# Optimization experiments

Hardware: AMD Instinct MI355X
Metric: run time of the kernel (lower is better)

## Reference

```python
import jax, jax.numpy as jnp
import numpy as np

N = 8192        # nodes in batch
E = 262144      # edges (avg degree 32)
IN_C = 64
OUT_C = 64
K = 3           # max_k
G = 64          # graphs in batch
NC = 10         # n_class
EPS = 1e-5      # batchnorm eps


def setup_inputs() -> dict:
    key = jax.random.key(0)
    ks = jax.random.split(key, 16)
    D_in = IN_C * K    # 192
    D_out = OUT_C * K  # 192
    inp = {
        'x': jax.random.normal(ks[0], (N, IN_C), jnp.float32),
        'edge_index': jax.random.randint(ks[1], (2, E), 0, N, dtype=jnp.int64),
        'batch': jnp.sort(jax.random.randint(ks[2], (N,), 0, G, dtype=jnp.int64)),
        # spectral-normed masked linear
        'W_orig': jax.random.normal(ks[3], (D_out, D_in), jnp.float32) * 0.05,
        'b': jnp.zeros((D_out,), jnp.float32),
        'u': jax.random.normal(ks[4], (D_out,), jnp.float32),
        # batchnorms (training-mode batch stats)
        'bn1_gamma': jnp.ones((D_out,), jnp.float32),
        'bn1_beta': jnp.zeros((D_out,), jnp.float32),
        'bn2_gamma': jnp.ones((D_out * 3,), jnp.float32),
        'bn2_beta': jnp.zeros((D_out * 3,), jnp.float32),
        # funnel head
        'w1': jax.random.normal(ks[5], (D_out * 2, D_out * 3), jnp.float32) * 0.05,
        'b1': jnp.zeros((D_out * 2,), jnp.float32),
        'w2': jax.random.normal(ks[6], (D_out, D_out * 2), jnp.float32) * 0.05,
        'b2': jnp.zeros((D_out,), jnp.float32),
        'w3': jax.random.normal(ks[7], (NC, D_out), jnp.float32) * 0.05,
        'b3': jnp.zeros((NC,), jnp.float32),
    }
    return inp


def _forward(x, edge_index, batch, W_orig, b, u, bn1_gamma, bn1_beta,
             bn2_gamma, bn2_beta, w1, b1, w2, b2, w3, b3):
    n = x.shape[0]
    row, col = edge_index[0], edge_index[1]
    # sym-normalized Laplacian L = I - D^-1/2 A D^-1/2, densified ([N,N])
    deg = jnp.zeros((n,), x.dtype).at[row].add(1.0)
    dinv = jnp.where(deg > 0, jax.lax.rsqrt(jnp.maximum(deg, 1.0)), 0.0)
    vals = -dinv[row] * dinv[col]
    L = jnp.zeros((n, n), x.dtype).at[row, col].add(vals)
    idx = jnp.arange(n)
    L = L.at[idx, idx].add(1.0)
    Hs = [x]
    h = x
    for _ in range(K - 1):
        h = L @ h
        Hs.append(h)
    Hcat = jnp.concatenate(Hs, axis=1)              # [N, IN_C*K]
    # spectral norm of W (one power-iteration step with stored u)
    v = W_orig.T @ u
    v = v / (jnp.linalg.norm(v) + 1e-12)
    sigma = u @ (W_orig @ v)
    W = W_orig / sigma
    # block lower-triangular mask: block i passes first IN_C*(i+1) input cols
    col_idx = jnp.arange(IN_C * K)
    row_block = jnp.arange(OUT_C * K) // OUT_C
    mask = (col_idx[None, :] < IN_C * (row_block[:, None] + 1)).astype(W.dtype)
    H = Hcat @ (W * mask).T + b                     # masked linear
    # reservoir_act_fun is identity (default)
    mu, var = H.mean(0), H.var(0)                   # BN (batch stats)
    H = bn1_gamma * (H - mu) * jax.lax.rsqrt(var + EPS) + bn1_beta
    # fused-style triple pooling over graph ids
    Hsum = jax.ops.segment_sum(H, batch, num_segments=G)
    cnt = jax.ops.segment_sum(jnp.ones((n,), H.dtype), batch, num_segments=G)
    Havg = Hsum / jnp.maximum(cnt, 1.0)[:, None]
    Hmax = jax.ops.segment_max(H, batch, num_segments=G)
    Hg = jnp.concatenate([Havg, Hsum, Hmax], axis=1)  # [G, 3*OUT_C*K]
    mu2, var2 = Hg.mean(0), Hg.var(0)
    xo = bn2_gamma * (Hg - mu2) * jax.lax.rsqrt(var2 + EPS) + bn2_beta
    # funnel output (dropout = identity in eval)
    xo = jax.nn.relu(xo @ w1.T + b1)
    xo = jax.nn.relu(xo @ w2.T + b2)
    return jax.nn.log_softmax(xo @ w3.T + b3, axis=1)


def reference(x, edge_index, batch, W_orig, b, u, bn1_gamma, bn1_beta,
              bn2_gamma, bn2_beta, w1, b1, w2, b2, w3, b3):
    return _forward(x, edge_index, batch, W_orig, b, u, bn1_gamma, bn1_beta,
                    bn2_gamma, bn2_beta, w1, b1, w2, b2, w3, b3)
```

## Files before the change

### kernel.cpp

```cpp
#include <hip/hip_runtime.h>
#include <math.h>

#define NN   8192
#define EE   262144
#define CIN  64
#define DD   192
#define GG   64
#define NCLS 10
#define D3   576
#define F1   384
#define F2   192
#define EPSB 1e-5f
#define NB   64
#define EPB  (EE / NB)
#define PS   8

__global__ __launch_bounds__(1024) void prep_kernel(const float* __restrict__ W,
    const float* __restrict__ u, const float* __restrict__ w1,
    const float* __restrict__ w2, const int* __restrict__ batch,
    float* __restrict__ sig, int* __restrict__ gstart,
    float* __restrict__ Wp, float* __restrict__ Wp1, float* __restrict__ Wp2) {
    int b = blockIdx.x, t = threadIdx.x;
    if (b < 324) {
        int idx = b * 1024 + t;
        if (idx < DD * DD) {
            int r = idx / DD, c = idx - r * DD;
            float m = (c < CIN * ((r >> 6) + 1)) ? 1.f : 0.f;
            Wp[((c >> 2) * DD + r) * 4 + (c & 3)] = m * W[idx];
        } else if (idx < DD * DD + F1 * D3) {
            int i1 = idx - DD * DD;
            int tt = i1 / D3, k = i1 - tt * D3;
            Wp1[((k >> 2) * F1 + tt) * 4 + (k & 3)] = w1[i1];
        } else {
            int i2 = idx - DD * DD - F1 * D3;
            int tt = i2 / F1, k = i2 - tt * F1;
            Wp2[((k >> 2) * F2 + tt) * 4 + (k & 3)] = w2[i2];
        }
        return;
    }
    if (b == 325) {
        for (int i = t; i < NN; i += 1024) {
            int b0 = batch[i];
            int b1 = (i + 1 < NN) ? batch[i + 1] : GG;
            if (i == 0) { for (int g = 0; g <= b0; g++) gstart[g] = 0; }
            for (int g = b0 + 1; g <= b1; g++) gstart[g] = i + 1;
        }
        return;
    }
    __shared__ float vp[768];
    __shared__ float vsh[DD];
    __shared__ float red[1024];
    if (t < 768) {
        int c = t >> 2, j = t & 3;
        float s = 0.f;
        const float* Wc = W + c;
        for (int i = j * 48; i < j * 48 + 48; i++) s += Wc[i * DD] * u[i];
        vp[t] = s;
    }
    __syncthreads();
    float vv = 0.f;
    if (t < DD) {
        float v = vp[4 * t] + vp[4 * t + 1] + vp[4 * t + 2] + vp[4 * t + 3];
        vsh[t] = v;
        vv = v * v;
    }
    red[t] = vv;
    __syncthreads();
    for (int off = 512; off > 0; off >>= 1) {
        if (t < off) red[t] += red[t + off];
        __syncthreads();
    }
    float norm = sqrtf(red[0]) + 1e-12f;
    __syncthreads();
    float a = 0.f;
    for (int idx = t; idx < DD * DD; idx += 1024) {
        int r = idx / DD, c = idx - r * DD;
        a += u[r] * W[idx] * vsh[c];
    }
    red[t] = a;
    __syncthreads();
    for (int off = 512; off > 0; off >>= 1) {
        if (t < off) red[t] += red[t + off];
        __syncthreads();
    }
    if (t == 0) sig[0] = norm / red[0];
}

__global__ __launch_bounds__(1024) void count_kernel(const int* __restrict__ ei,
                                                     int* __restrict__ pcnt) {
    __shared__ int hist[NN];
    int b = blockIdx.x, t = threadIdx.x;
    int4* hz = (int4*)hist;
    for (int i = t; i < NN / 4; i += 1024) hz[i] = make_int4(0, 0, 0, 0);
    __syncthreads();
    int e0 = b * EPB;
    for (int i = t; i < EPB; i += 1024) atomicAdd(&hist[ei[e0 + i]], 1);
    __syncthreads();
    const int4* hs = (const int4*)hist;
    int4* p4 = (int4*)&pcnt[b * NN];
    for (int i = t; i < NN / 4; i += 1024) p4[i] = hs[i];
}

__global__ __launch_bounds__(256) void offs_kernel(int* __restrict__ pcnt,
                                                   int* __restrict__ deg,
                                                   float* __restrict__ dinv) {
    int i = blockIdx.x * 256 + threadIdx.x;
    int run = 0;
#pragma unroll
    for (int b = 0; b < NB; b++) {
        int v = pcnt[b * NN + i];
        pcnt[b * NN + i] = run;
        run += v;
    }
    deg[i] = run;
    dinv[i] = (run > 0) ? rsqrtf((float)run) : 0.f;
}

__global__ __launch_bounds__(1024) void scatter_kernel(const int* __restrict__ ei,
                                                       const int* __restrict__ deg,
                                                       const int* __restrict__ off,
                                                       int* __restrict__ rowptr,
                                                       unsigned short* __restrict__ csr_col) {
    __shared__ int cur[NN];
    __shared__ int temp[1024];
    int b = blockIdx.x, t = threadIdx.x;
    int base = t * 8;
    int d[8], l[8];
    {
        const int4 a4 = *(const int4*)&deg[base];
        const int4 b4 = *(const int4*)&deg[base + 4];
        d[0] = a4.x; d[1] = a4.y; d[2] = a4.z; d[3] = a4.w;
        d[4] = b4.x; d[5] = b4.y; d[6] = b4.z; d[7] = b4.w;
    }
    int run = 0;
#pragma unroll
    for (int j = 0; j < 8; j++) { l[j] = run; run += d[j]; }
    temp[t] = run;
    __syncthreads();
    for (int o = 1; o < 1024; o <<= 1) {
        int v = (t >= o) ? temp[t - o] : 0;
        __syncthreads();
        temp[t] += v;
        __syncthreads();
    }
    int prefix = (t > 0) ? temp[t - 1] : 0;
    const int* ob = &off[b * NN];
#pragma unroll
    for (int j = 0; j < 8; j++) cur[base + j] = prefix + l[j] + ob[base + j];
    if (b == 0) {
#pragma unroll
        for (int j = 0; j < 8; j++) rowptr[base + j] = prefix + l[j];
        if (t == 1023) rowptr[NN] = temp[1023];
    }
    __syncthreads();
    int e0 = b * EPB;
    for (int i = t; i < EPB; i += 1024) {
        int r = ei[e0 + i];
        int c = ei[EE + e0 + i];
        int pos = atomicAdd(&cur[r], 1);
        csr_col[pos] = (unsigned short)c;
    }
}

__global__ __launch_bounds__(256) void spmm_kernel(const float* __restrict__ hin,
    int in_stride, int in_off,
    const int* __restrict__ rowptr, const unsigned short* __restrict__ col,
    const float* __restrict__ dinv,
    float* __restrict__ Hcat, int coff, int write_self) {
    int idx = blockIdx.x * 256 + threadIdx.x;
    int row = idx >> 6;
    int lane = idx & 63;
    int s = rowptr[row], e = rowptr[row + 1];
    float acc0 = 0.f, acc1 = 0.f;
    int p = s;
    for (; p + 1 < e; p += 2) {
        int c0 = col[p], c1 = col[p + 1];
        acc0 += dinv[c0] * hin[c0 * in_stride + in_off + lane];
        acc1 += dinv[c1] * hin[c1 * in_stride + in_off + lane];
    }
    if (p < e) {
        int c = col[p];
        acc0 += dinv[c] * hin[c * in_stride + in_off + lane];
    }
    float acc = acc0 + acc1;
    float self = hin[row * in_stride + in_off + lane];
    Hcat[row * DD + coff + lane] = self - dinv[row] * acc;
    if (write_self) Hcat[row * DD + lane] = self;
}

__global__ __launch_bounds__(192) void gemm_kernel(float* __restrict__ Hcat,
    const float* __restrict__ Wp, const float* __restrict__ bias,
    const float* __restrict__ sig) {
    __shared__ float hs[16 * DD];
    int t = threadIdx.x;
    int n0 = blockIdx.x * 16;
    const float4* src = (const float4*)&Hcat[n0 * DD];
    float4* dst = (float4*)hs;
#pragma unroll
    for (int i = 0; i < 4; i++) dst[t + 192 * i] = src[t + 192 * i];
    __syncthreads();
    float acc[16];
#pragma unroll
    for (int r = 0; r < 16; r++) acc[r] = 0.f;
    const float4* Wp4 = (const float4*)Wp;
    for (int k4 = 0; k4 < DD / 4; k4++) {
        float4 w = Wp4[k4 * DD + t];
#pragma unroll
        for (int r = 0; r < 16; r++) {
            const float4 h = *(const float4*)&hs[r * DD + k4 * 4];
            acc[r] += h.x * w.x + h.y * w.y + h.z * w.z + h.w * w.w;
        }
    }
    float inv_sigma = sig[0];
    float bv = bias[t];
#pragma unroll
    for (int r = 0; r < 16; r++) Hcat[(n0 + r) * DD + t] = inv_sigma * acc[r] + bv;
}

__global__ __launch_bounds__(192) void pool_kernel(const float* __restrict__ H,
    const int* __restrict__ gstart,
    float* __restrict__ Psum, float* __restrict__ Psq,
    float* __restrict__ Pmin, float* __restrict__ Pmax) {
    int b = blockIdx.x;
    int g = b >> 3, s = b & 7, c = threadIdx.x;
    int beg = gstart[g], end = gstart[g + 1];
    float sum = 0.f, sq = 0.f, mn = INFINITY, mx = -INFINITY;
    for (int i = beg + s; i < end; i += PS) {
        float x = H[i * DD + c];
        sum += x; sq += x * x;
        mn = fminf(mn, x); mx = fmaxf(mx, x);
    }
    Psum[b * DD + c] = sum; Psq[b * DD + c] = sq;
    Pmin[b * DD + c] = mn;  Pmax[b * DD + c] = mx;
}

__global__ __launch_bounds__(64) void hg_kernel(
    const float* __restrict__ Psum, const float* __restrict__ Psq,
    const float* __restrict__ Pmin, const float* __restrict__ Pmax,
    const int* __restrict__ gstart,
    const float* __restrict__ g1, const float* __restrict__ be1,
    const float* __restrict__ g2, const float* __restrict__ be2,
    float* __restrict__ Hg) {
    int t = blockIdx.x;
    int g = threadIdx.x;
    int f = t / DD, c = t - f * DD;
    float Sg = 0.f, Qg = 0.f;
#pragma unroll
    for (int s = 0; s < PS; s++) {
        Sg += Psum[(g * PS + s) * DD + c];
        Qg += Psq[(g * PS + s) * DD + c];
    }
    float S = Sg, Q = Qg;
    for (int off = 32; off > 0; off >>= 1) {
        S += __shfl_xor(S, off);
        Q += __shfl_xor(Q, off);
    }
    float mu = S * (1.f / (float)NN);
    float var = Q * (1.f / (float)NN) - mu * mu;
    float sc = g1[c] * rsqrtf(var + EPSB);
    float bb = be1[c];
    float v;
    if (f == 2) {
        float mx = -INFINITY, mn = INFINITY;
#pragma unroll
        for (int s = 0; s < PS; s++) {
            mx = fmaxf(mx, Pmax[(g * PS + s) * DD + c]);
            mn = fminf(mn, Pmin[(g * PS + s) * DD + c]);
        }
        float raw = (sc >= 0.f) ? mx : mn;
        v = sc * (raw - mu) + bb;
    } else {
        float nf = (float)(gstart[g + 1] - gstart[g]);
        float hsum = sc * (Sg - nf * mu) + nf * bb;
        v = (f == 0) ? hsum / fmaxf(nf, 1.f) : hsum;
    }
    float s2 = v, ss2 = v * v;
    for (int off = 32; off > 0; off >>= 1) {
        s2 += __shfl_xor(s2, off);
        ss2 += __shfl_xor(ss2, off);
    }
    float m2 = s2 * (1.f / (float)GG);
    float var2 = ss2 * (1.f / (float)GG) - m2 * m2;
    float sc2 = g2[t] * rsqrtf(var2 + EPSB);
    Hg[g * D3 + t] = sc2 * (v - m2) + be2[t];
}

__global__ __launch_bounds__(F1) void funnel_kernel(const float* __restrict__ Hg,
    const float* __restrict__ Wp1, const float* __restrict__ b1,
    const float* __restrict__ Wp2, const float* __restrict__ b2,
    const float* __restrict__ w3, const float* __restrict__ b3,
    float* __restrict__ out) {
    __shared__ float hg[D3];
    __shared__ float x1[F1];
    __shared__ float x2[F2];
    __shared__ float lg[NCLS];
    __shared__ float s_lse;
    int g = blockIdx.x, t = threadIdx.x;
    for (int i = t; i < D3; i += F1) hg[i] = Hg[g * D3 + i];
    __syncthreads();
    {
        float a = b1[t];
        const float4* W4 = (const float4*)Wp1;
        for (int k4 = 0; k4 < D3 / 4; k4++) {
            float4 w = W4[k4 * F1 + t];
            const float4 h = *(const float4*)&hg[k4 * 4];
            a += w.x * h.x + w.y * h.y + w.z * h.z + w.w * h.w;
        }
        x1[t] = fmaxf(a, 0.f);
    }
    __syncthreads();
    if (t < F2) {
        float a = b2[t];
        const float4* W4 = (const float4*)Wp2;
        for (int k4 = 0; k4 < F1 / 4; k4++) {
            float4 w = W4[k4 * F2 + t];
            const float4 h = *(const float4*)&x1[k4 * 4];
            a += w.x * h.x + w.y * h.y + w.z * h.z + w.w * h.w;
        }
        x2[t] = fmaxf(a, 0.f);
    }
    __syncthreads();
    if (t < NCLS) {
        float a = b3[t];
        const float4* wr = (const float4*)&w3[t * F2];
        const float4* h4 = (const float4*)x2;
        for (int k = 0; k < F2 / 4; k++) {
            float4 w = wr[k], h = h4[k];
            a += w.x * h.x + w.y * h.y + w.z * h.z + w.w * h.w;
        }
        lg[t] = a;
    }
    __syncthreads();
    if (t == 0) {
        float m = lg[0];
        for (int i = 1; i < NCLS; i++) m = fmaxf(m, lg[i]);
        float se = 0.f;
        for (int i = 0; i < NCLS; i++) se += expf(lg[i] - m);
        s_lse = m + logf(se);
    }
    __syncthreads();
    if (t < NCLS) out[g * NCLS + t] = lg[t] - s_lse;
}


extern "C" void kernel_launch(void* const* d_in, const int* in_sizes, int n_in,
                              void* d_out, int out_size, void* d_ws, size_t ws_size,
                              hipStream_t stream) {
    (void)in_sizes; (void)n_in; (void)out_size; (void)ws_size;
    const float* x     = (const float*)d_in[0];
    const int*   ei    = (const int*)d_in[1];
    const int*   batch = (const int*)d_in[2];
    const float* W     = (const float*)d_in[3];
    const float* b     = (const float*)d_in[4];
    const float* u     = (const float*)d_in[5];
    const float* g1    = (const float*)d_in[6];
    const float* be1   = (const float*)d_in[7];
    const float* g2    = (const float*)d_in[8];
    const float* be2   = (const float*)d_in[9];
    const float* w1    = (const float*)d_in[10];
    const float* b1    = (const float*)d_in[11];
    const float* w2    = (const float*)d_in[12];
    const float* b2    = (const float*)d_in[13];
    const float* w3    = (const float*)d_in[14];
    const float* b3    = (const float*)d_in[15];
    float* out = (float*)d_out;
    char*  ws  = (char*)d_ws;

    int*            gstart  = (int*)(ws + 0);
    int*            rowptr  = (int*)(ws + 512);
    int*            deg     = (int*)(ws + 33536);
    float*          dinv    = (float*)(ws + 66304);
    float*          sig     = (float*)(ws + 99072);
    float*          Wp      = (float*)(ws + 99328);
    float*          Psum    = (float*)(ws + 246784);
    float*          Psq     = (float*)(ws + 640000);
    float*          Pmin    = (float*)(ws + 1033216);
    float*          Pmax    = (float*)(ws + 1426432);
    float*          Hg      = (float*)(ws + 1819648);
    unsigned short* csr_col = (unsigned short*)(ws + 1967104);
    float*          Wp1     = (float*)(ws + 2491392);
    float*          Wp2     = (float*)(ws + 3376128);
    int*            pcnt    = (int*)(ws + 3671040);
    float*          Hcat    = (float*)(ws + 5768192);

    prep_kernel<<<326, 1024, 0, stream>>>(W, u, w1, w2, batch, sig, gstart, Wp, Wp1, Wp2);
    count_kernel<<<NB, 1024, 0, stream>>>(ei, pcnt);
    offs_kernel<<<NN / 256, 256, 0, stream>>>(pcnt, deg, dinv);
    scatter_kernel<<<NB, 1024, 0, stream>>>(ei, deg, pcnt, rowptr, csr_col);
    spmm_kernel<<<NN * 64 / 256, 256, 0, stream>>>(x, CIN, 0, rowptr, csr_col, dinv, Hcat, CIN, 1);
    spmm_kernel<<<NN * 64 / 256, 256, 0, stream>>>(Hcat, DD, CIN, rowptr, csr_col, dinv, Hcat, 2 * CIN, 0);
    gemm_kernel<<<NN / 16, 192, 0, stream>>>(Hcat, Wp, b, sig);
    pool_kernel<<<GG * PS, 192, 0, stream>>>(Hcat, gstart, Psum, Psq, Pmin, Pmax);
    hg_kernel<<<D3, 64, 0, stream>>>(Psum, Psq, Pmin, Pmax, gstart, g1, be1, g2, be2, Hg);
    funnel_kernel<<<GG, F1, 0, stream>>>(Hg, Wp1, b1, Wp2, b2, w3, b3, out);
}
```

Before: 203.9 us.

## Fold edge histogram into prep kernel and compute offsets inside scatter

Moves the per-block edge-count histogram into extra blocks of the prep kernel so it runs alongside the weight preprocessing. The separate offsets kernel is dropped, and each scatter block now sums all 64 partial histograms itself to get degrees and its own block prefix, writing dinv from block 0. This removes two kernel launches and their serialization. In exchange, every prep block now reserves 32KB of shared memory, which may lower prep occupancy, and each scatter block rereads the full 2MB partial-count array.

```diff
diff --git a/kernel.cpp b/kernel.cpp
--- a/kernel.cpp
+++ b/kernel.cpp
@@ -18,8 +18,10 @@
 __global__ __launch_bounds__(1024) void prep_kernel(const float* __restrict__ W,
     const float* __restrict__ u, const float* __restrict__ w1,
     const float* __restrict__ w2, const int* __restrict__ batch,
-    float* __restrict__ sig, int* __restrict__ gstart,
+    const int* __restrict__ ei,
+    float* __restrict__ sig, int* __restrict__ gstart, int* __restrict__ pcnt,
     float* __restrict__ Wp, float* __restrict__ Wp1, float* __restrict__ Wp2) {
+    __shared__ int hist[NN];
     int b = blockIdx.x, t = threadIdx.x;
     if (b < 324) {
         int idx = b * 1024 + t;
@@ -47,9 +49,22 @@
         }
         return;
     }
-    __shared__ float vp[768];
-    __shared__ float vsh[DD];
-    __shared__ float red[1024];
+    if (b >= 326) {
+        int cb = b - 326;
+        int4* hz = (int4*)hist;
+        for (int i = t; i < NN / 4; i += 1024) hz[i] = make_int4(0, 0, 0, 0);
+        __syncthreads();
+        int e0 = cb * EPB;
+        for (int i = t; i < EPB; i += 1024) atomicAdd(&hist[ei[e0 + i]], 1);
+        __syncthreads();
+        const int4* hs = (const int4*)hist;
+        int4* p4 = (int4*)&pcnt[cb * NN];
+        for (int i = t; i < NN / 4; i += 1024) p4[i] = hs[i];
+        return;
+    }
+    float* vp  = (float*)hist;
+    float* vsh = vp + 768;
+    float* red = vsh + DD;
     if (t < 768) {
         int c = t >> 2, j = t & 3;
         float s = 0.f;
@@ -86,52 +101,28 @@
     if (t == 0) sig[0] = norm / red[0];
 }
 
-__global__ __launch_bounds__(1024) void count_kernel(const int* __restrict__ ei,
-                                                     int* __restrict__ pcnt) {
-    __shared__ int hist[NN];
-    int b = blockIdx.x, t = threadIdx.x;
-    int4* hz = (int4*)hist;
-    for (int i = t; i < NN / 4; i += 1024) hz[i] = make_int4(0, 0, 0, 0);
-    __syncthreads();
-    int e0 = b * EPB;
-    for (int i = t; i < EPB; i += 1024) atomicAdd(&hist[ei[e0 + i]], 1);
-    __syncthreads();
-    const int4* hs = (const int4*)hist;
-    int4* p4 = (int4*)&pcnt[b * NN];
-    for (int i = t; i < NN / 4; i += 1024) p4[i] = hs[i];
-}
-
-__global__ __launch_bounds__(256) void offs_kernel(int* __restrict__ pcnt,
-                                                   int* __restrict__ deg,
-                                                   float* __restrict__ dinv) {
-    int i = blockIdx.x * 256 + threadIdx.x;
-    int run = 0;
-#pragma unroll
-    for (int b = 0; b < NB; b++) {
-        int v = pcnt[b * NN + i];
-        pcnt[b * NN + i] = run;
-        run += v;
-    }
-    deg[i] = run;
-    dinv[i] = (run > 0) ? rsqrtf((float)run) : 0.f;
-}
-
 __global__ __launch_bounds__(1024) void scatter_kernel(const int* __restrict__ ei,
-                                                       const int* __restrict__ deg,
-                                                       const int* __restrict__ off,
+                                                       const int* __restrict__ pcnt,
                                                        int* __restrict__ rowptr,
+                                                       float* __restrict__ dinv,
                                                        unsigned short* __restrict__ csr_col) {
     __shared__ int cur[NN];
     __shared__ int temp[1024];
     int b = blockIdx.x, t = threadIdx.x;
     int base = t * 8;
-    int d[8], l[8];
-    {
-        const int4 a4 = *(const int4*)&deg[base];
-        const int4 b4 = *(const int4*)&deg[base + 4];
-        d[0] = a4.x; d[1] = a4.y; d[2] = a4.z; d[3] = a4.w;
-        d[4] = b4.x; d[5] = b4.y; d[6] = b4.z; d[7] = b4.w;
-    }
+    int d[8] = {0,0,0,0,0,0,0,0};
+    int of[8] = {0,0,0,0,0,0,0,0};
+    for (int bb = 0; bb < NB; bb++) {
+        const int4 a4 = *(const int4*)&pcnt[bb * NN + base];
+        const int4 b4 = *(const int4*)&pcnt[bb * NN + base + 4];
+        if (bb < b) {
+            of[0] += a4.x; of[1] += a4.y; of[2] += a4.z; of[3] += a4.w;
+            of[4] += b4.x; of[5] += b4.y; of[6] += b4.z; of[7] += b4.w;
+        }
+        d[0] += a4.x; d[1] += a4.y; d[2] += a4.z; d[3] += a4.w;
+        d[4] += b4.x; d[5] += b4.y; d[6] += b4.z; d[7] += b4.w;
+    }
+    int l[8];
     int run = 0;
 #pragma unroll
     for (int j = 0; j < 8; j++) { l[j] = run; run += d[j]; }
@@ -144,12 +135,14 @@
         __syncthreads();
     }
     int prefix = (t > 0) ? temp[t - 1] : 0;
-    const int* ob = &off[b * NN];
-#pragma unroll
-    for (int j = 0; j < 8; j++) cur[base + j] = prefix + l[j] + ob[base + j];
+#pragma unroll
+    for (int j = 0; j < 8; j++) cur[base + j] = prefix + l[j] + of[j];
     if (b == 0) {
 #pragma unroll
-        for (int j = 0; j < 8; j++) rowptr[base + j] = prefix + l[j];
+        for (int j = 0; j < 8; j++) {
+            rowptr[base + j] = prefix + l[j];
+            dinv[base + j] = (d[j] > 0) ? rsqrtf((float)d[j]) : 0.f;
+        }
         if (t == 1023) rowptr[NN] = temp[1023];
     }
     __syncthreads();
@@ -368,7 +361,6 @@
 
     int*            gstart  = (int*)(ws + 0);
     int*            rowptr  = (int*)(ws + 512);
-    int*            deg     = (int*)(ws + 33536);
     float*          dinv    = (float*)(ws + 66304);
     float*          sig     = (float*)(ws + 99072);
     float*          Wp      = (float*)(ws + 99328);
@@ -383,10 +375,9 @@
     int*            pcnt    = (int*)(ws + 3671040);
     float*          Hcat    = (float*)(ws + 5768192);
 
-    prep_kernel<<<326, 1024, 0, stream>>>(W, u, w1, w2, batch, sig, gstart, Wp, Wp1, Wp2);
-    count_kernel<<<NB, 1024, 0, stream>>>(ei, pcnt);
-    offs_kernel<<<NN / 256, 256, 0, stream>>>(pcnt, deg, dinv);
-    scatter_kernel<<<NB, 1024, 0, stream>>>(ei, deg, pcnt, rowptr, csr_col);
+    prep_kernel<<<326 + NB, 1024, 0, stream>>>(W, u, w1, w2, batch, ei,
+                                               sig, gstart, pcnt, Wp, Wp1, Wp2);
+    scatter_kernel<<<NB, 1024, 0, stream>>>(ei, pcnt, rowptr, dinv, csr_col);
     spmm_kernel<<<NN * 64 / 256, 256, 0, stream>>>(x, CIN, 0, rowptr, csr_col, dinv, Hcat, CIN, 1);
     spmm_kernel<<<NN * 64 / 256, 256, 0, stream>>>(Hcat, DD, CIN, rowptr, csr_col, dinv, Hcat, 2 * CIN, 0);
     gemm_kernel<<<NN / 16, 192, 0, stream>>>(Hcat, Wp, b, sig);
```

Measured after the change: 214.4 us. +5.1%, slower.
